# Kernel tuning notes

Hardware: AMD Instinct MI355X
Metric: run time of the kernel (lower is better)

## Reference

```python
import jax, jax.numpy as jnp
import numpy as np

N, E = 100000, 1600000
IN, HID, NCLS = 128, 128, 64


def setup_inputs() -> dict:
    key = jax.random.key(0)
    ks = jax.random.split(key, 8)
    x = jax.random.normal(ks[0], (N, IN), jnp.float32)
    edge_index = jax.random.randint(ks[1], (2, E), 0, N, dtype=jnp.int32)
    s1 = 1.0 / np.sqrt(IN)
    s2 = 1.0 / np.sqrt(HID)
    return {
        "x": x,
        "edge_index": edge_index,
        "Wl1": jax.random.uniform(ks[2], (IN, HID), jnp.float32, -s1, s1),
        "Wr1": jax.random.uniform(ks[3], (IN, HID), jnp.float32, -s1, s1),
        "b1": jnp.zeros((HID,), jnp.float32),
        "Wl2": jax.random.uniform(ks[4], (HID, NCLS), jnp.float32, -s2, s2),
        "Wr2": jax.random.uniform(ks[5], (HID, NCLS), jnp.float32, -s2, s2),
        "b2": jnp.zeros((NCLS,), jnp.float32),
    }


def _sage_conv(x, src, dst, inv_deg, Wl, Wr, b):
    # mean-aggregate neighbor features at each destination node (PyG SAGEConv)
    agg = jax.ops.segment_sum(x[src], dst, num_segments=N)  # [N, d]
    agg = agg * inv_deg[:, None]
    # out = lin_l(mean_j x_j) + lin_r(x_i); bias lives in lin_l
    return agg @ Wl + x @ Wr + b


def reference(x, edge_index, Wl1, Wr1, b1, Wl2, Wr2, b2):
    src, dst = edge_index[0], edge_index[1]
    deg = jax.ops.segment_sum(jnp.ones((E,), jnp.float32), dst, num_segments=N)
    inv_deg = 1.0 / jnp.maximum(deg, 1.0)
    h = _sage_conv(x, src, dst, inv_deg, Wl1, Wr1, b1)
    h = jax.nn.relu(h)
    # dropout is identity at inference (training=False)
    h = _sage_conv(h, src, dst, inv_deg, Wl2, Wr2, b2)
    return jax.nn.log_softmax(h, axis=1)
```

## Files before the change

kernel.cpp:

```cpp
#include <hip/hip_runtime.h>
#include <hip/hip_bf16.h>


typedef __attribute__((ext_vector_type(8))) short short8;
typedef __attribute__((ext_vector_type(4))) float f32x4;
typedef __attribute__((ext_vector_type(2))) float f32x2;

#define NPB 512
#define BCAP 16384
#define CHUNK 8192

__device__ __forceinline__ ushort f2bf(float f) {
    unsigned u = __float_as_uint(f);
    return (ushort)((u + 0x7fff + ((u >> 16) & 1)) >> 16);
}
__device__ __forceinline__ float bflo(unsigned v) { return __uint_as_float(v << 16); }
__device__ __forceinline__ float bfhi(unsigned v) { return __uint_as_float(v & 0xffff0000u); }
__device__ __forceinline__ unsigned pk4bf(float a, float b) {
    unsigned r;
    asm("v_cvt_pk_bf16_f32 %0, %1, %2" : "=v"(r) : "v"(a), "v"(b));
    return r;
}
__device__ __forceinline__ f32x2 shflx2(f32x2 v, int m) {
    f32x2 r; r[0] = __shfl_xor(v[0], m); r[1] = __shfl_xor(v[1], m); return r;
}

__device__ __forceinline__ void wfrag_one(const float* W, ushort* Wf, int i, int COLS) {
    int j = i & 7, m = (i >> 3) & 15, kc = (i >> 7) & 15, ct = i >> 11;
    Wf[i] = f2bf(W[(kc * 8 + j) * COLS + ct * 16 + m]);
}

__global__ void __launch_bounds__(256)
k1_scatter_cvtw(const int* __restrict__ src, const int* __restrict__ dst,
                int* __restrict__ bcount, unsigned* __restrict__ bbuf, int E, int NSC,
                const float* __restrict__ Wl1, const float* __restrict__ Wr1,
                const float* __restrict__ Wl2, const float* __restrict__ Wr2,
                ushort* __restrict__ Wf_l1, ushort* __restrict__ Wf_r1,
                ushort* __restrict__ Wf_l2, ushort* __restrict__ Wf_r2) {
    int tid = threadIdx.x;
    if ((int)blockIdx.x >= NSC) {
        int i = ((int)blockIdx.x - NSC) * 256 + tid;
        if (i < 16384)       wfrag_one(Wl1, Wf_l1, i, 128);
        else if (i < 32768)  wfrag_one(Wr1, Wf_r1, i - 16384, 128);
        else if (i < 40960)  wfrag_one(Wl2, Wf_l2, i - 32768, 64);
        else if (i < 49152)  wfrag_one(Wr2, Wf_r2, i - 40960, 64);
        return;
    }
    __shared__ unsigned entry[CHUNK];
    __shared__ unsigned char ebkt[CHUNK];
    __shared__ int lhist[256], lbase[256], lcur[256];
    lhist[tid] = 0;
    __syncthreads();
    int e0 = blockIdx.x * CHUNK;
    int cnt = min(CHUNK, E - e0);
    int nv = cnt >> 2;
    for (int t = tid; t < nv; t += 256) {
        int4 d4 = ((const int4*)(dst + e0))[t];
        int4 s4 = ((const int4*)(src + e0))[t];
        int i = t * 4;
        int b0 = d4.x >> 9, b1 = d4.y >> 9, b2 = d4.z >> 9, b3 = d4.w >> 9;
        entry[i + 0] = ((unsigned)s4.x << 9) | (unsigned)(d4.x & 511);
        entry[i + 1] = ((unsigned)s4.y << 9) | (unsigned)(d4.y & 511);
        entry[i + 2] = ((unsigned)s4.z << 9) | (unsigned)(d4.z & 511);
        entry[i + 3] = ((unsigned)s4.w << 9) | (unsigned)(d4.w & 511);
        ebkt[i + 0] = (unsigned char)b0; ebkt[i + 1] = (unsigned char)b1;
        ebkt[i + 2] = (unsigned char)b2; ebkt[i + 3] = (unsigned char)b3;
        atomicAdd(&lhist[b0], 1); atomicAdd(&lhist[b1], 1);
        atomicAdd(&lhist[b2], 1); atomicAdd(&lhist[b3], 1);
    }
    for (int i = (nv << 2) + tid; i < cnt; i += 256) {
        int d = dst[e0 + i], s = src[e0 + i];
        int b = d >> 9;
        entry[i] = ((unsigned)s << 9) | (unsigned)(d & 511);
        ebkt[i] = (unsigned char)b;
        atomicAdd(&lhist[b], 1);
    }
    __syncthreads();
    int h = lhist[tid];
    lbase[tid] = (h > 0) ? atomicAdd(&bcount[tid], h) : 0;
    lcur[tid] = 0;
    __syncthreads();
    for (int i = tid; i < cnt; i += 256) {
        int b = ebkt[i];
        int o = atomicAdd(&lcur[b], 1);
        bbuf[(long)b * BCAP + lbase[b] + o] = entry[i];
    }
}

template <int CTOT>
__device__ __forceinline__ void stage_weights(const ushort* __restrict__ Wfl,
                                              const ushort* __restrict__ Wfr,
                                              ushort* dst, int tid) {
    constexpr int HALF = CTOT / 2;
    constexpr int ITERS = (CTOT * 2) / 8192;
#pragma unroll
    for (int r = 0; r < ITERS; ++r) {
        int u = r * 4096 + tid * 8;
        const ushort* s = (u < HALF) ? (Wfl + u) : (Wfr + (u - HALF));
        *(short8*)(dst + u) = *(const short8*)s;
    }
}

template <int COLS, bool F32IN>
__device__ __forceinline__ void proj_body(int bid, int tid,
                            const void* __restrict__ xin,
                            const ushort* __restrict__ Wfl, const ushort* __restrict__ Wfr,
                            const float* __restrict__ bias,
                            unsigned char* __restrict__ p8, ushort* __restrict__ q, int N,
                            ushort* wsm) {
    constexpr int CT = COLS / 16;
    stage_weights<2 * COLS * 128>(Wfl, Wfr, wsm, tid);
    __syncthreads();
    const ushort* Wl = wsm;
    const ushort* Wr = wsm + COLS * 128;

    int wave = tid >> 6, lane = tid & 63;
    int quad = lane >> 4, m = lane & 15;
    long row0 = (long)bid * 128 + wave * 16;
    long node = row0 + m;
    long arow = (node < N) ? node : (N - 1);

    f32x4 accp[CT], accq[CT];
#pragma unroll
    for (int ct = 0; ct < CT; ++ct) { accp[ct] = (f32x4)0.0f; accq[ct] = (f32x4)0.0f; }

#pragma unroll
    for (int kk = 0; kk < 128; kk += 32) {
        short8 b;
        if (F32IN) {
            const float* xf = (const float*)xin + arow * 128 + kk + quad * 8;
            float4 f0 = *(const float4*)xf;
            float4 f1 = *(const float4*)(xf + 4);
            union { short8 s; unsigned u[4]; } bu;
            bu.u[0] = pk4bf(f0.x, f0.y);
            bu.u[1] = pk4bf(f0.z, f0.w);
            bu.u[2] = pk4bf(f1.x, f1.y);
            bu.u[3] = pk4bf(f1.z, f1.w);
            b = bu.s;
        } else {
            b = *(const short8*)((const ushort*)xin + arow * 128 + kk + quad * 8);
        }
        int kc = (kk >> 3) + quad;
#pragma unroll
        for (int ct = 0; ct < CT; ++ct) {
            int boff = ((ct * 16 + kc) * 16 + m) * 8;
            short8 al = *(const short8*)(Wl + boff);
            short8 ar = *(const short8*)(Wr + boff);
            accp[ct] = __builtin_amdgcn_mfma_f32_16x16x32_bf16(al, b, accp[ct], 0, 0, 0);
            accq[ct] = __builtin_amdgcn_mfma_f32_16x16x32_bf16(ar, b, accq[ct], 0, 0, 0);
        }
    }

    if (node <= N) {
        unsigned msk = (node == N) ? 0u : ~0u;
#pragma unroll
        for (int ct = 0; ct < CT; ++ct) {
            int c0 = ct * 16 + quad * 4;
            float4 bv = *(const float4*)(bias + c0);
            float q0 = accq[ct][0] + bv.x, q1 = accq[ct][1] + bv.y;
            float q2 = accq[ct][2] + bv.z, q3 = accq[ct][3] + bv.w;
            unsigned w = (unsigned)__builtin_amdgcn_cvt_pk_fp8_f32(accp[ct][0], accp[ct][1], 0, false);
            w = (unsigned)__builtin_amdgcn_cvt_pk_fp8_f32(accp[ct][2], accp[ct][3], (int)w, true);
            *(unsigned*)(p8 + node * COLS + c0) = w & msk;
            uint2 qw; qw.x = pk4bf(q0, q1) & msk; qw.y = pk4bf(q2, q3) & msk;
            *(uint2*)(q + node * COLS + c0) = qw;
        }
    }
}

__global__ void __launch_bounds__(512, 4)
k2_csr_proj1(const unsigned* __restrict__ bbuf, const int* __restrict__ bcount,
             int* __restrict__ rsd,
             float* __restrict__ inv_deg, int* __restrict__ ssrc, int NBcsr, int N,
             const float* __restrict__ x,
             const ushort* __restrict__ Wfl, const ushort* __restrict__ Wfr,
             const float* __restrict__ bias,
             unsigned char* __restrict__ p8, ushort* __restrict__ q) {
    extern __shared__ char smem[];
    int tid = threadIdx.x;
    if ((int)blockIdx.x >= NBcsr) {
        proj_body<128, true>((int)blockIdx.x - NBcsr, tid, x, Wfl, Wfr, bias, p8, q, N,
                             (ushort*)smem);
        return;
    }
    int* sdeg = (int*)smem;
    int* lcur = sdeg + NPB;
    int* wsum = lcur + NPB;
    unsigned* ecache = (unsigned*)(wsum + 16);
    const int ECAPV = 3836;
    int b = blockIdx.x;
    int node0 = b * NPB;
    sdeg[tid] = 0;
    __syncthreads();
    int cnt = bcount[b];
    long base = (long)b * BCAP;
    const unsigned* bb = bbuf + base;
    int nv = cnt >> 2;
    int cnv = min(nv, ECAPV);
    for (int t = tid; t < nv; t += 512) {
        uint4 e = ((const uint4*)bb)[t];
        if (t < cnv) ((uint4*)ecache)[t] = e;
        atomicAdd(&sdeg[e.x & 511], 1);
        atomicAdd(&sdeg[e.y & 511], 1);
        atomicAdd(&sdeg[e.z & 511], 1);
        atomicAdd(&sdeg[e.w & 511], 1);
    }
    for (int i = (nv << 2) + tid; i < cnt; i += 512)
        atomicAdd(&sdeg[bb[i] & 511], 1);
    __syncthreads();
    int lane = tid & 63, wv = tid >> 6;
    int c0 = sdeg[tid];
    int dp = (c0 + 15) & ~15;
    int v = dp;
#pragma unroll
    for (int o = 1; o < 64; o <<= 1) {
        int t = __shfl_up(v, o);
        if (lane >= o) v += t;
    }
    if (lane == 63) wsum[wv] = v;
    __syncthreads();
    int add = 0;
    for (int w = 0; w < wv; ++w) add += wsum[w];
    int rs0 = v + add - dp;
    lcur[tid] = rs0;
    if (node0 + tid < N) {
        int2 rv; rv.x = (int)(base + rs0); rv.y = dp;
        *(int2*)(rsd + 2 * (node0 + tid)) = rv;
        inv_deg[node0 + tid] = 1.0f / (float)(c0 > 1 ? c0 : 1);
    }
    __syncthreads();
    for (int t = tid; t < cnv; t += 512) {
        uint4 e = ((const uint4*)ecache)[t];
        int p0 = atomicAdd(&lcur[e.x & 511], 1);
        int p1 = atomicAdd(&lcur[e.y & 511], 1);
        int p2 = atomicAdd(&lcur[e.z & 511], 1);
        int p3 = atomicAdd(&lcur[e.w & 511], 1);
        ssrc[base + p0] = (int)(e.x >> 9);
        ssrc[base + p1] = (int)(e.y >> 9);
        ssrc[base + p2] = (int)(e.z >> 9);
        ssrc[base + p3] = (int)(e.w >> 9);
    }
    for (int t = cnv + tid; t < nv; t += 512) {
        uint4 e = ((const uint4*)bb)[t];
        int p0 = atomicAdd(&lcur[e.x & 511], 1);
        int p1 = atomicAdd(&lcur[e.y & 511], 1);
        int p2 = atomicAdd(&lcur[e.z & 511], 1);
        int p3 = atomicAdd(&lcur[e.w & 511], 1);
        ssrc[base + p0] = (int)(e.x >> 9);
        ssrc[base + p1] = (int)(e.y >> 9);
        ssrc[base + p2] = (int)(e.z >> 9);
        ssrc[base + p3] = (int)(e.w >> 9);
    }
    for (int i = (nv << 2) + tid; i < cnt; i += 512) {
        unsigned w = bb[i];
        int pos = atomicAdd(&lcur[w & 511], 1);
        ssrc[base + pos] = (int)(w >> 9);
    }
    for (int i = c0; i < dp; ++i) ssrc[base + rs0 + i] = N;
    if (tid == 511) {
        int tot = v + add;
        for (int k = 0; k < 16; ++k) ssrc[base + tot + k] = N;
    }
}

__global__ void __launch_bounds__(256)
agg_relu_kernel(const unsigned char* __restrict__ p8,
                const ushort* __restrict__ q,
                const int* __restrict__ ssrc,
                const int* __restrict__ rsd,
                const float* __restrict__ inv_deg,
                ushort* __restrict__ hb, int N) {
    int wave = threadIdx.x >> 6, lane = threadIdx.x & 63;
    int nA = blockIdx.x * 8 + wave * 2;
    if (nA >= N) return;
    int nB = nA + 1;
    bool hasB = (nB < N);
    int g = lane >> 4, lm = lane & 15;
    int2 rvA = *(const int2*)(rsd + 2 * nA);
    int2 rvB = hasB ? *(const int2*)(rsd + 2 * nB) : make_int2(rvA.x, 0);
    int dpA = rvA.y, dpB = rvB.y;
    float ivA = inv_deg[nA];
    float ivB = hasB ? inv_deg[nB] : 0.f;
    uint4 qvA = make_uint4(0u,0u,0u,0u), qvB = make_uint4(0u,0u,0u,0u);
    if (g == 0) {
        qvA = *(const uint4*)(q + (long)nA * 128 + lm * 8);
        if (hasB) qvB = *(const uint4*)(q + (long)nB * 128 + lm * 8);
    }
    const int* spA = ssrc + rvA.x;
    const int* spB = ssrc + rvB.x;
    const unsigned char* pb = p8 + lm * 8;
    f32x2 aA0=(f32x2)0.f, aA1=(f32x2)0.f, aA2=(f32x2)0.f, aA3=(f32x2)0.f;
    f32x2 aB0=(f32x2)0.f, aB1=(f32x2)0.f, aB2=(f32x2)0.f, aB3=(f32x2)0.f;
    int4 sA = *(const int4*)(spA + 4 * g);
    int4 sB = *(const int4*)(spB + 4 * g);
    int dmin = min(dpA, dpB);
    int j = 0;
    for (; j < dmin; j += 16) {
        uint2 a0 = *(const uint2*)(pb + (unsigned)sA.x * 128u);
        uint2 a1 = *(const uint2*)(pb + (unsigned)sA.y * 128u);
        uint2 a2 = *(const uint2*)(pb + (unsigned)sA.z * 128u);
        uint2 a3 = *(const uint2*)(pb + (unsigned)sA.w * 128u);
        uint2 b0 = *(const uint2*)(pb + (unsigned)sB.x * 128u);
        uint2 b1 = *(const uint2*)(pb + (unsigned)sB.y * 128u);
        uint2 b2 = *(const uint2*)(pb + (unsigned)sB.z * 128u);
        uint2 b3 = *(const uint2*)(pb + (unsigned)sB.w * 128u);
        sA = *(const int4*)(spA + j + 16 + 4 * g);
        sB = *(const int4*)(spB + j + 16 + 4 * g);
        aA0 += __builtin_amdgcn_cvt_pk_f32_fp8((int)a0.x, false);
        aA1 += __builtin_amdgcn_cvt_pk_f32_fp8((int)a0.x, true);
        aA2 += __builtin_amdgcn_cvt_pk_f32_fp8((int)a0.y, false);
        aA3 += __builtin_amdgcn_cvt_pk_f32_fp8((int)a0.y, true);
        aA0 += __builtin_amdgcn_cvt_pk_f32_fp8((int)a1.x, false);
        aA1 += __builtin_amdgcn_cvt_pk_f32_fp8((int)a1.x, true);
        aA2 += __builtin_amdgcn_cvt_pk_f32_fp8((int)a1.y, false);
        aA3 += __builtin_amdgcn_cvt_pk_f32_fp8((int)a1.y, true);
        aA0 += __builtin_amdgcn_cvt_pk_f32_fp8((int)a2.x, false);
        aA1 += __builtin_amdgcn_cvt_pk_f32_fp8((int)a2.x, true);
        aA2 += __builtin_amdgcn_cvt_pk_f32_fp8((int)a2.y, false);
        aA3 += __builtin_amdgcn_cvt_pk_f32_fp8((int)a2.y, true);
        aA0 += __builtin_amdgcn_cvt_pk_f32_fp8((int)a3.x, false);
        aA1 += __builtin_amdgcn_cvt_pk_f32_fp8((int)a3.x, true);
        aA2 += __builtin_amdgcn_cvt_pk_f32_fp8((int)a3.y, false);
        aA3 += __builtin_amdgcn_cvt_pk_f32_fp8((int)a3.y, true);
        aB0 += __builtin_amdgcn_cvt_pk_f32_fp8((int)b0.x, false);
        aB1 += __builtin_amdgcn_cvt_pk_f32_fp8((int)b0.x, true);
        aB2 += __builtin_amdgcn_cvt_pk_f32_fp8((int)b0.y, false);
        aB3 += __builtin_amdgcn_cvt_pk_f32_fp8((int)b0.y, true);
        aB0 += __builtin_amdgcn_cvt_pk_f32_fp8((int)b1.x, false);
        aB1 += __builtin_amdgcn_cvt_pk_f32_fp8((int)b1.x, true);
        aB2 += __builtin_amdgcn_cvt_pk_f32_fp8((int)b1.y, false);
        aB3 += __builtin_amdgcn_cvt_pk_f32_fp8((int)b1.y, true);
        aB0 += __builtin_amdgcn_cvt_pk_f32_fp8((int)b2.x, false);
        aB1 += __builtin_amdgcn_cvt_pk_f32_fp8((int)b2.x, true);
        aB2 += __builtin_amdgcn_cvt_pk_f32_fp8((int)b2.y, false);
        aB3 += __builtin_amdgcn_cvt_pk_f32_fp8((int)b2.y, true);
        aB0 += __builtin_amdgcn_cvt_pk_f32_fp8((int)b3.x, false);
        aB1 += __builtin_amdgcn_cvt_pk_f32_fp8((int)b3.x, true);
        aB2 += __builtin_amdgcn_cvt_pk_f32_fp8((int)b3.y, false);
        aB3 += __builtin_amdgcn_cvt_pk_f32_fp8((int)b3.y, true);
    }
    for (; j < dpA; j += 16) {
        uint2 a0 = *(const uint2*)(pb + (unsigned)sA.x * 128u);
        uint2 a1 = *(const uint2*)(pb + (unsigned)sA.y * 128u);
        uint2 a2 = *(const uint2*)(pb + (unsigned)sA.z * 128u);
        uint2 a3 = *(const uint2*)(pb + (unsigned)sA.w * 128u);
        sA = *(const int4*)(spA + j + 16 + 4 * g);
        aA0 += __builtin_amdgcn_cvt_pk_f32_fp8((int)a0.x, false);
        aA1 += __builtin_amdgcn_cvt_pk_f32_fp8((int)a0.x, true);
        aA2 += __builtin_amdgcn_cvt_pk_f32_fp8((int)a0.y, false);
        aA3 += __builtin_amdgcn_cvt_pk_f32_fp8((int)a0.y, true);
        aA0 += __builtin_amdgcn_cvt_pk_f32_fp8((int)a1.x, false);
        aA1 += __builtin_amdgcn_cvt_pk_f32_fp8((int)a1.x, true);
        aA2 += __builtin_amdgcn_cvt_pk_f32_fp8((int)a1.y, false);
        aA3 += __builtin_amdgcn_cvt_pk_f32_fp8((int)a1.y, true);
        aA0 += __builtin_amdgcn_cvt_pk_f32_fp8((int)a2.x, false);
        aA1 += __builtin_amdgcn_cvt_pk_f32_fp8((int)a2.x, true);
        aA2 += __builtin_amdgcn_cvt_pk_f32_fp8((int)a2.y, false);
        aA3 += __builtin_amdgcn_cvt_pk_f32_fp8((int)a2.y, true);
        aA0 += __builtin_amdgcn_cvt_pk_f32_fp8((int)a3.x, false);
        aA1 += __builtin_amdgcn_cvt_pk_f32_fp8((int)a3.x, true);
        aA2 += __builtin_amdgcn_cvt_pk_f32_fp8((int)a3.y, false);
        aA3 += __builtin_amdgcn_cvt_pk_f32_fp8((int)a3.y, true);
    }
    for (; j < dpB; j += 16) {
        uint2 b0 = *(const uint2*)(pb + (unsigned)sB.x * 128u);
        uint2 b1 = *(const uint2*)(pb + (unsigned)sB.y * 128u);
        uint2 b2 = *(const uint2*)(pb + (unsigned)sB.z * 128u);
        uint2 b3 = *(const uint2*)(pb + (unsigned)sB.w * 128u);
        sB = *(const int4*)(spB + j + 16 + 4 * g);
        aB0 += __builtin_amdgcn_cvt_pk_f32_fp8((int)b0.x, false);
        aB1 += __builtin_amdgcn_cvt_pk_f32_fp8((int)b0.x, true);
        aB2 += __builtin_amdgcn_cvt_pk_f32_fp8((int)b0.y, false);
        aB3 += __builtin_amdgcn_cvt_pk_f32_fp8((int)b0.y, true);
        aB0 += __builtin_amdgcn_cvt_pk_f32_fp8((int)b1.x, false);
        aB1 += __builtin_amdgcn_cvt_pk_f32_fp8((int)b1.x, true);
        aB2 += __builtin_amdgcn_cvt_pk_f32_fp8((int)b1.y, false);
        aB3 += __builtin_amdgcn_cvt_pk_f32_fp8((int)b1.y, true);
        aB0 += __builtin_amdgcn_cvt_pk_f32_fp8((int)b2.x, false);
        aB1 += __builtin_amdgcn_cvt_pk_f32_fp8((int)b2.x, true);
        aB2 += __builtin_amdgcn_cvt_pk_f32_fp8((int)b2.y, false);
        aB3 += __builtin_amdgcn_cvt_pk_f32_fp8((int)b2.y, true);
        aB0 += __builtin_amdgcn_cvt_pk_f32_fp8((int)b3.x, false);
        aB1 += __builtin_amdgcn_cvt_pk_f32_fp8((int)b3.x, true);
        aB2 += __builtin_amdgcn_cvt_pk_f32_fp8((int)b3.y, false);
        aB3 += __builtin_amdgcn_cvt_pk_f32_fp8((int)b3.y, true);
    }
    aA0 += shflx2(aA0, 16); aA1 += shflx2(aA1, 16);
    aA2 += shflx2(aA2, 16); aA3 += shflx2(aA3, 16);
    aB0 += shflx2(aB0, 16); aB1 += shflx2(aB1, 16);
    aB2 += shflx2(aB2, 16); aB3 += shflx2(aB3, 16);
    aA0 += shflx2(aA0, 32); aA1 += shflx2(aA1, 32);
    aA2 += shflx2(aA2, 32); aA3 += shflx2(aA3, 32);
    aB0 += shflx2(aB0, 32); aB1 += shflx2(aB1, 32);
    aB2 += shflx2(aB2, 32); aB3 += shflx2(aB3, 32);
    if (g == 0) {
        float h0 = fmaxf(aA0[0] * ivA + bflo(qvA.x), 0.f);
        float h1 = fmaxf(aA0[1] * ivA + bfhi(qvA.x), 0.f);
        float h2 = fmaxf(aA1[0] * ivA + bflo(qvA.y), 0.f);
        float h3 = fmaxf(aA1[1] * ivA + bfhi(qvA.y), 0.f);
        float h4 = fmaxf(aA2[0] * ivA + bflo(qvA.z), 0.f);
        float h5 = fmaxf(aA2[1] * ivA + bfhi(qvA.z), 0.f);
        float h6 = fmaxf(aA3[0] * ivA + bflo(qvA.w), 0.f);
        float h7 = fmaxf(aA3[1] * ivA + bfhi(qvA.w), 0.f);
        uint4 hw;
        hw.x = pk4bf(h0, h1); hw.y = pk4bf(h2, h3);
        hw.z = pk4bf(h4, h5); hw.w = pk4bf(h6, h7);
        *(uint4*)(hb + (long)nA * 128 + lm * 8) = hw;
        if (hasB) {
            float g0 = fmaxf(aB0[0] * ivB + bflo(qvB.x), 0.f);
            float g1 = fmaxf(aB0[1] * ivB + bfhi(qvB.x), 0.f);
            float g2 = fmaxf(aB1[0] * ivB + bflo(qvB.y), 0.f);
            float g3 = fmaxf(aB1[1] * ivB + bfhi(qvB.y), 0.f);
            float g4 = fmaxf(aB2[0] * ivB + bflo(qvB.z), 0.f);
            float g5 = fmaxf(aB2[1] * ivB + bfhi(qvB.z), 0.f);
            float g6 = fmaxf(aB3[0] * ivB + bflo(qvB.w), 0.f);
            float g7 = fmaxf(aB3[1] * ivB + bfhi(qvB.w), 0.f);
            uint4 gw;
            gw.x = pk4bf(g0, g1); gw.y = pk4bf(g2, g3);
            gw.z = pk4bf(g4, g5); gw.w = pk4bf(g6, g7);
            *(uint4*)(hb + (long)nB * 128 + lm * 8) = gw;
        }
    }
}

__global__ void __launch_bounds__(512, 4)
proj2_kernel(const ushort* __restrict__ hb,
             const ushort* __restrict__ Wfl, const ushort* __restrict__ Wfr,
             const float* __restrict__ bias,
             unsigned char* __restrict__ u8, ushort* __restrict__ v, int N) {
    __shared__ ushort wsm[2 * 64 * 128];
    proj_body<64, false>((int)blockIdx.x, (int)threadIdx.x, hb, Wfl, Wfr, bias, u8, v, N,
                         wsm);
}

__global__ void __launch_bounds__(256)
agg_lsm_kernel(const unsigned char* __restrict__ u8,
               const ushort* __restrict__ v,
               const int* __restrict__ ssrc,
               const int* __restrict__ rsd,
               const float* __restrict__ inv_deg,
               float* __restrict__ out, int N) {
    int wave = threadIdx.x >> 6, lane = threadIdx.x & 63;
    int nA = blockIdx.x * 8 + wave * 2;
    if (nA >= N) return;
    int nB = nA + 1;
    bool hasB = (nB < N);
    int g = lane >> 4, lm = lane & 15;
    int2 rvA = *(const int2*)(rsd + 2 * nA);
    int2 rvB = hasB ? *(const int2*)(rsd + 2 * nB) : make_int2(rvA.x, 0);
    int dpA = rvA.y, dpB = rvB.y;
    float ivA = inv_deg[nA];
    float ivB = hasB ? inv_deg[nB] : 0.f;
    uint2 vvA = *(const uint2*)(v + (long)nA * 64 + lm * 4);
    uint2 vvB = hasB ? *(const uint2*)(v + (long)nB * 64 + lm * 4) : make_uint2(0u,0u);
    const int* spA = ssrc + rvA.x;
    const int* spB = ssrc + rvB.x;
    const unsigned char* ub = u8 + lm * 4;
    f32x2 aA0=(f32x2)0.f, aA1=(f32x2)0.f, aB0=(f32x2)0.f, aB1=(f32x2)0.f;
    int4 sA = *(const int4*)(spA + 4 * g);
    int4 sB = *(const int4*)(spB + 4 * g);
    int dmin = min(dpA, dpB);
    int j = 0;
    for (; j < dmin; j += 16) {
        unsigned a0 = *(const unsigned*)(ub + (unsigned)sA.x * 64u);
        unsigned a1 = *(const unsigned*)(ub + (unsigned)sA.y * 64u);
        unsigned a2 = *(const unsigned*)(ub + (unsigned)sA.z * 64u);
        unsigned a3 = *(const unsigned*)(ub + (unsigned)sA.w * 64u);
        unsigned b0 = *(const unsigned*)(ub + (unsigned)sB.x * 64u);
        unsigned b1 = *(const unsigned*)(ub + (unsigned)sB.y * 64u);
        unsigned b2 = *(const unsigned*)(ub + (unsigned)sB.z * 64u);
        unsigned b3 = *(const unsigned*)(ub + (unsigned)sB.w * 64u);
        sA = *(const int4*)(spA + j + 16 + 4 * g);
        sB = *(const int4*)(spB + j + 16 + 4 * g);
        aA0 += __builtin_amdgcn_cvt_pk_f32_fp8((int)a0, false);
        aA1 += __builtin_amdgcn_cvt_pk_f32_fp8((int)a0, true);
        aA0 += __builtin_amdgcn_cvt_pk_f32_fp8((int)a1, false);
        aA1 += __builtin_amdgcn_cvt_pk_f32_fp8((int)a1, true);
        aA0 += __builtin_amdgcn_cvt_pk_f32_fp8((int)a2, false);
        aA1 += __builtin_amdgcn_cvt_pk_f32_fp8((int)a2, true);
        aA0 += __builtin_amdgcn_cvt_pk_f32_fp8((int)a3, false);
        aA1 += __builtin_amdgcn_cvt_pk_f32_fp8((int)a3, true);
        aB0 += __builtin_amdgcn_cvt_pk_f32_fp8((int)b0, false);
        aB1 += __builtin_amdgcn_cvt_pk_f32_fp8((int)b0, true);
        aB0 += __builtin_amdgcn_cvt_pk_f32_fp8((int)b1, false);
        aB1 += __builtin_amdgcn_cvt_pk_f32_fp8((int)b1, true);
        aB0 += __builtin_amdgcn_cvt_pk_f32_fp8((int)b2, false);
        aB1 += __builtin_amdgcn_cvt_pk_f32_fp8((int)b2, true);
        aB0 += __builtin_amdgcn_cvt_pk_f32_fp8((int)b3, false);
        aB1 += __builtin_amdgcn_cvt_pk_f32_fp8((int)b3, true);
    }
    for (; j < dpA; j += 16) {
        unsigned a0 = *(const unsigned*)(ub + (unsigned)sA.x * 64u);
        unsigned a1 = *(const unsigned*)(ub + (unsigned)sA.y * 64u);
        unsigned a2 = *(const unsigned*)(ub + (unsigned)sA.z * 64u);
        unsigned a3 = *(const unsigned*)(ub + (unsigned)sA.w * 64u);
        sA = *(const int4*)(spA + j + 16 + 4 * g);
        aA0 += __builtin_amdgcn_cvt_pk_f32_fp8((int)a0, false);
        aA1 += __builtin_amdgcn_cvt_pk_f32_fp8((int)a0, true);
        aA0 += __builtin_amdgcn_cvt_pk_f32_fp8((int)a1, false);
        aA1 += __builtin_amdgcn_cvt_pk_f32_fp8((int)a1, true);
        aA0 += __builtin_amdgcn_cvt_pk_f32_fp8((int)a2, false);
        aA1 += __builtin_amdgcn_cvt_pk_f32_fp8((int)a2, true);
        aA0 += __builtin_amdgcn_cvt_pk_f32_fp8((int)a3, false);
        aA1 += __builtin_amdgcn_cvt_pk_f32_fp8((int)a3, true);
    }
    for (; j < dpB; j += 16) {
        unsigned b0 = *(const unsigned*)(ub + (unsigned)sB.x * 64u);
        unsigned b1 = *(const unsigned*)(ub + (unsigned)sB.y * 64u);
        unsigned b2 = *(const unsigned*)(ub + (unsigned)sB.z * 64u);
        unsigned b3 = *(const unsigned*)(ub + (unsigned)sB.w * 64u);
        sB = *(const int4*)(spB + j + 16 + 4 * g);
        aB0 += __builtin_amdgcn_cvt_pk_f32_fp8((int)b0, false);
        aB1 += __builtin_amdgcn_cvt_pk_f32_fp8((int)b0, true);
        aB0 += __builtin_amdgcn_cvt_pk_f32_fp8((int)b1, false);
        aB1 += __builtin_amdgcn_cvt_pk_f32_fp8((int)b1, true);
        aB0 += __builtin_amdgcn_cvt_pk_f32_fp8((int)b2, false);
        aB1 += __builtin_amdgcn_cvt_pk_f32_fp8((int)b2, true);
        aB0 += __builtin_amdgcn_cvt_pk_f32_fp8((int)b3, false);
        aB1 += __builtin_amdgcn_cvt_pk_f32_fp8((int)b3, true);
    }
    aA0 += shflx2(aA0, 16); aA1 += shflx2(aA1, 16);
    aB0 += shflx2(aB0, 16); aB1 += shflx2(aB1, 16);
    aA0 += shflx2(aA0, 32); aA1 += shflx2(aA1, 32);
    aB0 += shflx2(aB0, 32); aB1 += shflx2(aB1, 32);

    float zA0 = aA0[0] * ivA + bflo(vvA.x), zA1 = aA0[1] * ivA + bfhi(vvA.x);
    float zA2 = aA1[0] * ivA + bflo(vvA.y), zA3 = aA1[1] * ivA + bfhi(vvA.y);
    float zB0 = aB0[0] * ivB + bflo(vvB.x), zB1 = aB0[1] * ivB + bfhi(vvB.x);
    float zB2 = aB1[0] * ivB + bflo(vvB.y), zB3 = aB1[1] * ivB + bfhi(vvB.y);
    float mA = fmaxf(fmaxf(zA0, zA1), fmaxf(zA2, zA3));
    float mB = fmaxf(fmaxf(zB0, zB1), fmaxf(zB2, zB3));
#pragma unroll
    for (int o = 8; o > 0; o >>= 1) {
        mA = fmaxf(mA, __shfl_xor(mA, o));
        mB = fmaxf(mB, __shfl_xor(mB, o));
    }
    float eA = (__expf(zA0 - mA) + __expf(zA1 - mA)) + (__expf(zA2 - mA) + __expf(zA3 - mA));
    float eB = (__expf(zB0 - mB) + __expf(zB1 - mB)) + (__expf(zB2 - mB) + __expf(zB3 - mB));
#pragma unroll
    for (int o = 8; o > 0; o >>= 1) {
        eA += __shfl_xor(eA, o);
        eB += __shfl_xor(eB, o);
    }
    float lsA = mA + __logf(eA);
    float lsB = mB + __logf(eB);
    if (g == 0) {
        float4 oA;
        oA.x = zA0 - lsA; oA.y = zA1 - lsA; oA.z = zA2 - lsA; oA.w = zA3 - lsA;
        *(float4*)(out + (long)nA * 64 + lm * 4) = oA;
        if (hasB) {
            float4 oB;
            oB.x = zB0 - lsB; oB.y = zB1 - lsB; oB.z = zB2 - lsB; oB.w = zB3 - lsB;
            *(float4*)(out + (long)nB * 64 + lm * 4) = oB;
        }
    }
}

extern "C" void kernel_launch(void* const* d_in, const int* in_sizes, int n_in,
                              void* d_out, int out_size, void* d_ws, size_t ws_size,
                              hipStream_t stream) {
    const float* x   = (const float*)d_in[0];
    const int*   ei  = (const int*)d_in[1];
    const float* Wl1 = (const float*)d_in[2];
    const float* Wr1 = (const float*)d_in[3];
    const float* b1  = (const float*)d_in[4];
    const float* Wl2 = (const float*)d_in[5];
    const float* Wr2 = (const float*)d_in[6];
    const float* b2  = (const float*)d_in[7];

    const int N = in_sizes[0] / 128;
    const int E = in_sizes[1] / 2;
    const int* src = ei;
    const int* dst = ei + E;
    const int NB = (N + NPB - 1) / NPB;
    const int NSC = (E + CHUNK - 1) / CHUNK;

    size_t off = 0;
    auto take = [&](size_t nbytes) -> void* {
        void* ptr = (void*)((char*)d_ws + off);
        off += (nbytes + 255) & ~(size_t)255;
        return ptr;
    };
    int*      bcount    = (int*)take((size_t)NB * 4);
    unsigned* bbuf      = (unsigned*)take((size_t)NB * BCAP * 4);
    int*      rsd       = (int*)take((size_t)N * 8);
    float*    inv_deg   = (float*)take((size_t)N * 4);
    int*      ssrc      = (int*)take((size_t)NB * BCAP * 4);
    unsigned char* p8   = (unsigned char*)take((size_t)(N + 1) * 128);
    ushort*   q         = (ushort*)take((size_t)(N + 1) * 128 * 2);
    ushort*   hb        = (ushort*)take((size_t)N * 128 * 2);
    ushort*   Wf_l1     = (ushort*)take(128 * 128 * 2);
    ushort*   Wf_r1     = (ushort*)take(128 * 128 * 2);
    ushort*   Wf_l2     = (ushort*)take(64 * 128 * 2);
    ushort*   Wf_r2     = (ushort*)take(64 * 128 * 2);
    unsigned char* u8 = p8;
    ushort*        v  = q;
    (void)ws_size; (void)n_in; (void)out_size;

    static bool attr_set = false;
    if (!attr_set) {
        hipFuncSetAttribute((const void*)k2_csr_proj1,
                            hipFuncAttributeMaxDynamicSharedMemorySize, 65536);
        attr_set = true;
    }

    hipMemsetAsync(bcount, 0, (size_t)NB * 4, stream);

    k1_scatter_cvtw<<<NSC + 192, 256, 0, stream>>>(src, dst, bcount, bbuf, E, NSC,
                                                   Wl1, Wr1, Wl2, Wr2,
                                                   Wf_l1, Wf_r1, Wf_l2, Wf_r2);

    int P1 = (N + 127) / 128;
    k2_csr_proj1<<<NB + P1, 512, 65536, stream>>>(bbuf, bcount, rsd, inv_deg,
                                                  ssrc, NB, N, x, Wf_l1, Wf_r1, b1, p8, q);

    agg_relu_kernel<<<(N + 7) / 8, 256, 0, stream>>>(p8, q, ssrc, rsd, inv_deg, hb, N);

    proj2_kernel<<<(N + 127) / 128, 512, 0, stream>>>(hb, Wf_l2, Wf_r2, b2, u8, v, N);
    agg_lsm_kernel<<<(N + 7) / 8, 256, 0, stream>>>(u8, v, ssrc, rsd, inv_deg,
                                                    (float*)d_out, N);
}
```

Before: 242.4 us.

## Fuse layer-1 aggregation with layer-2 projection and persist proj1 tiles

Merges the ReLU aggregation kernel with the second-layer projection. Each 512-thread block aggregates 16 nodes into shared memory and runs the bf16 MFMA for both weight matrices directly, so the hb intermediate never goes through global memory and one launch disappears. The layer-1 projection blocks become a persistent grid of 316 that stages the weights once and loops over tiles. The final aggregation now handles one node per wave instead of two. The trade-off is that weights are restaged into shared memory in every small fused block, and occupancy is lower because of the shared-memory footprint.

```diff
diff --git a/kernel.cpp b/kernel.cpp
--- a/kernel.cpp
+++ b/kernel.cpp
@@ -102,18 +102,12 @@
 }
 
 template <int COLS, bool F32IN>
-__device__ __forceinline__ void proj_body(int bid, int tid,
+__device__ __forceinline__ void proj_tile(int bid, int tid,
                             const void* __restrict__ xin,
-                            const ushort* __restrict__ Wfl, const ushort* __restrict__ Wfr,
+                            const ushort* Wl, const ushort* Wr,
                             const float* __restrict__ bias,
-                            unsigned char* __restrict__ p8, ushort* __restrict__ q, int N,
-                            ushort* wsm) {
+                            unsigned char* __restrict__ p8, ushort* __restrict__ q, int N) {
     constexpr int CT = COLS / 16;
-    stage_weights<2 * COLS * 128>(Wfl, Wfr, wsm, tid);
-    __syncthreads();
-    const ushort* Wl = wsm;
-    const ushort* Wr = wsm + COLS * 128;
-
     int wave = tid >> 6, lane = tid & 63;
     int quad = lane >> 4, m = lane & 15;
     long row0 = (long)bid * 128 + wave * 16;
@@ -171,7 +165,8 @@
 __global__ void __launch_bounds__(512, 4)
 k2_csr_proj1(const unsigned* __restrict__ bbuf, const int* __restrict__ bcount,
              int* __restrict__ rsd,
-             float* __restrict__ inv_deg, int* __restrict__ ssrc, int NBcsr, int N,
+             float* __restrict__ inv_deg, int* __restrict__ ssrc,
+             int NBcsr, int PGRID, int NT, int N,
              const float* __restrict__ x,
              const ushort* __restrict__ Wfl, const ushort* __restrict__ Wfr,
              const float* __restrict__ bias,
@@ -179,8 +174,11 @@
     extern __shared__ char smem[];
     int tid = threadIdx.x;
     if ((int)blockIdx.x >= NBcsr) {
-        proj_body<128, true>((int)blockIdx.x - NBcsr, tid, x, Wfl, Wfr, bias, p8, q, N,
-                             (ushort*)smem);
+        ushort* wsm = (ushort*)smem;
+        stage_weights<2 * 128 * 128>(Wfl, Wfr, wsm, tid);
+        __syncthreads();
+        for (int t = (int)blockIdx.x - NBcsr; t < NT; t += PGRID)
+            proj_tile<128, true>(t, tid, x, wsm, wsm + 128 * 128, bias, p8, q, N);
         return;
     }
     int* sdeg = (int*)smem;
@@ -263,28 +261,36 @@
     }
 }
 
-__global__ void __launch_bounds__(256)
-agg_relu_kernel(const unsigned char* __restrict__ p8,
-                const ushort* __restrict__ q,
-                const int* __restrict__ ssrc,
-                const int* __restrict__ rsd,
-                const float* __restrict__ inv_deg,
-                ushort* __restrict__ hb, int N) {
-    int wave = threadIdx.x >> 6, lane = threadIdx.x & 63;
-    int nA = blockIdx.x * 8 + wave * 2;
-    if (nA >= N) return;
-    int nB = nA + 1;
-    bool hasB = (nB < N);
+__global__ void __launch_bounds__(512, 6)
+agg_relu_proj2(const unsigned char* __restrict__ p8,
+               const ushort* __restrict__ q,
+               const int* __restrict__ ssrc,
+               const int* __restrict__ rsd,
+               const float* __restrict__ inv_deg,
+               const ushort* __restrict__ Wfl, const ushort* __restrict__ Wfr,
+               const float* __restrict__ bias,
+               unsigned char* __restrict__ u8,
+               ushort* __restrict__ v,
+               int N) {
+    __shared__ ushort wsm[2 * 64 * 128];
+    __shared__ ushort hs[16][136];
+    int tid = threadIdx.x;
+    stage_weights<2 * 64 * 128>(Wfl, Wfr, wsm, tid);
+
+    int wave = tid >> 6, lane = tid & 63;
+    int row0 = (int)blockIdx.x * 16;
+    int nA = row0 + wave * 2, nB = nA + 1;
+    int cA = (nA < N) ? nA : N - 1;
+    int cB = (nB < N) ? nB : N - 1;
     int g = lane >> 4, lm = lane & 15;
-    int2 rvA = *(const int2*)(rsd + 2 * nA);
-    int2 rvB = hasB ? *(const int2*)(rsd + 2 * nB) : make_int2(rvA.x, 0);
+    int2 rvA = *(const int2*)(rsd + 2 * cA);
+    int2 rvB = *(const int2*)(rsd + 2 * cB);
     int dpA = rvA.y, dpB = rvB.y;
-    float ivA = inv_deg[nA];
-    float ivB = hasB ? inv_deg[nB] : 0.f;
+    float ivA = inv_deg[cA], ivB = inv_deg[cB];
     uint4 qvA = make_uint4(0u,0u,0u,0u), qvB = make_uint4(0u,0u,0u,0u);
     if (g == 0) {
-        qvA = *(const uint4*)(q + (long)nA * 128 + lm * 8);
-        if (hasB) qvB = *(const uint4*)(q + (long)nB * 128 + lm * 8);
+        qvA = *(const uint4*)(q + (long)cA * 128 + lm * 8);
+        qvB = *(const uint4*)(q + (long)cB * 128 + lm * 8);
     }
     const int* spA = ssrc + rvA.x;
     const int* spB = ssrc + rvB.x;
@@ -402,35 +408,53 @@
         float h5 = fmaxf(aA2[1] * ivA + bfhi(qvA.z), 0.f);
         float h6 = fmaxf(aA3[0] * ivA + bflo(qvA.w), 0.f);
         float h7 = fmaxf(aA3[1] * ivA + bfhi(qvA.w), 0.f);
-        uint4 hw;
-        hw.x = pk4bf(h0, h1); hw.y = pk4bf(h2, h3);
-        hw.z = pk4bf(h4, h5); hw.w = pk4bf(h6, h7);
-        *(uint4*)(hb + (long)nA * 128 + lm * 8) = hw;
-        if (hasB) {
-            float g0 = fmaxf(aB0[0] * ivB + bflo(qvB.x), 0.f);
-            float g1 = fmaxf(aB0[1] * ivB + bfhi(qvB.x), 0.f);
-            float g2 = fmaxf(aB1[0] * ivB + bflo(qvB.y), 0.f);
-            float g3 = fmaxf(aB1[1] * ivB + bfhi(qvB.y), 0.f);
-            float g4 = fmaxf(aB2[0] * ivB + bflo(qvB.z), 0.f);
-            float g5 = fmaxf(aB2[1] * ivB + bfhi(qvB.z), 0.f);
-            float g6 = fmaxf(aB3[0] * ivB + bflo(qvB.w), 0.f);
-            float g7 = fmaxf(aB3[1] * ivB + bfhi(qvB.w), 0.f);
-            uint4 gw;
-            gw.x = pk4bf(g0, g1); gw.y = pk4bf(g2, g3);
-            gw.z = pk4bf(g4, g5); gw.w = pk4bf(g6, g7);
-            *(uint4*)(hb + (long)nB * 128 + lm * 8) = gw;
+        uint4 hwA;
+        hwA.x = pk4bf(h0, h1); hwA.y = pk4bf(h2, h3);
+        hwA.z = pk4bf(h4, h5); hwA.w = pk4bf(h6, h7);
+        *(uint4*)(&hs[wave * 2 + 0][lm * 8]) = hwA;
+        float g0 = fmaxf(aB0[0] * ivB + bflo(qvB.x), 0.f);
+        float g1 = fmaxf(aB0[1] * ivB + bfhi(qvB.x), 0.f);
+        float g2 = fmaxf(aB1[0] * ivB + bflo(qvB.y), 0.f);
+        float g3 = fmaxf(aB1[1] * ivB + bfhi(qvB.y), 0.f);
+        float g4 = fmaxf(aB2[0] * ivB + bflo(qvB.z), 0.f);
+        float g5 = fmaxf(aB2[1] * ivB + bfhi(qvB.z), 0.f);
+        float g6 = fmaxf(aB3[0] * ivB + bflo(qvB.w), 0.f);
+        float g7 = fmaxf(aB3[1] * ivB + bfhi(qvB.w), 0.f);
+        uint4 hwB;
+        hwB.x = pk4bf(g0, g1); hwB.y = pk4bf(g2, g3);
+        hwB.z = pk4bf(g4, g5); hwB.w = pk4bf(g6, g7);
+        *(uint4*)(&hs[wave * 2 + 1][lm * 8]) = hwB;
+    }
+    __syncthreads();
+    {
+        int mat = wave & 1, ct = wave >> 1;
+        const ushort* W = mat ? (wsm + 64 * 128) : wsm;
+        f32x4 acc = (f32x4)0.0f;
+#pragma unroll
+        for (int kk = 0; kk < 128; kk += 32) {
+            short8 bfr = *(const short8*)(&hs[lm][kk + g * 8]);
+            int kc = (kk >> 3) + g;
+            short8 afr = *(const short8*)(W + ((ct * 16 + kc) * 16 + lm) * 8);
+            acc = __builtin_amdgcn_mfma_f32_16x16x32_bf16(afr, bfr, acc, 0, 0, 0);
         }
-    }
-}
-
-__global__ void __launch_bounds__(512, 4)
-proj2_kernel(const ushort* __restrict__ hb,
-             const ushort* __restrict__ Wfl, const ushort* __restrict__ Wfr,
-             const float* __restrict__ bias,
-             unsigned char* __restrict__ u8, ushort* __restrict__ v, int N) {
-    __shared__ ushort wsm[2 * 64 * 128];
-    proj_body<64, false>((int)blockIdx.x, (int)threadIdx.x, hb, Wfl, Wfr, bias, u8, v, N,
-                         wsm);
+        int node = row0 + lm;
+        if (node < N) {
+            int c0 = ct * 16 + g * 4;
+            if (mat == 0) {
+                unsigned w = (unsigned)__builtin_amdgcn_cvt_pk_fp8_f32(acc[0], acc[1], 0, false);
+                w = (unsigned)__builtin_amdgcn_cvt_pk_fp8_f32(acc[2], acc[3], (int)w, true);
+                *(unsigned*)(u8 + (long)node * 64 + c0) = w;
+            } else {
+                float4 bv = *(const float4*)(bias + c0);
+                uint2 qw;
+                qw.x = pk4bf(acc[0] + bv.x, acc[1] + bv.y);
+                qw.y = pk4bf(acc[2] + bv.z, acc[3] + bv.w);
+                *(uint2*)(v + (long)node * 64 + c0) = qw;
+            }
+        }
+    }
+    if (blockIdx.x == 0 && tid < 16)
+        ((unsigned*)(u8 + (long)N * 64))[tid] = 0u;
 }
 
 __global__ void __launch_bounds__(256)
@@ -441,118 +465,48 @@
                const float* __restrict__ inv_deg,
                float* __restrict__ out, int N) {
     int wave = threadIdx.x >> 6, lane = threadIdx.x & 63;
-    int nA = blockIdx.x * 8 + wave * 2;
-    if (nA >= N) return;
-    int nB = nA + 1;
-    bool hasB = (nB < N);
+    int n = blockIdx.x * 4 + wave;
+    if (n >= N) return;
     int g = lane >> 4, lm = lane & 15;
-    int2 rvA = *(const int2*)(rsd + 2 * nA);
-    int2 rvB = hasB ? *(const int2*)(rsd + 2 * nB) : make_int2(rvA.x, 0);
-    int dpA = rvA.y, dpB = rvB.y;
-    float ivA = inv_deg[nA];
-    float ivB = hasB ? inv_deg[nB] : 0.f;
-    uint2 vvA = *(const uint2*)(v + (long)nA * 64 + lm * 4);
-    uint2 vvB = hasB ? *(const uint2*)(v + (long)nB * 64 + lm * 4) : make_uint2(0u,0u);
-    const int* spA = ssrc + rvA.x;
-    const int* spB = ssrc + rvB.x;
+    int2 rv = *(const int2*)(rsd + 2 * n);
+    int start = rv.x, dp = rv.y;
+    float iv = inv_deg[n];
+    uint2 vv2 = *(const uint2*)(v + (long)n * 64 + lm * 4);
+    const int* sp = ssrc + start;
     const unsigned char* ub = u8 + lm * 4;
-    f32x2 aA0=(f32x2)0.f, aA1=(f32x2)0.f, aB0=(f32x2)0.f, aB1=(f32x2)0.f;
-    int4 sA = *(const int4*)(spA + 4 * g);
-    int4 sB = *(const int4*)(spB + 4 * g);
-    int dmin = min(dpA, dpB);
-    int j = 0;
-    for (; j < dmin; j += 16) {
-        unsigned a0 = *(const unsigned*)(ub + (unsigned)sA.x * 64u);
-        unsigned a1 = *(const unsigned*)(ub + (unsigned)sA.y * 64u);
-        unsigned a2 = *(const unsigned*)(ub + (unsigned)sA.z * 64u);
-        unsigned a3 = *(const unsigned*)(ub + (unsigned)sA.w * 64u);
-        unsigned b0 = *(const unsigned*)(ub + (unsigned)sB.x * 64u);
-        unsigned b1 = *(const unsigned*)(ub + (unsigned)sB.y * 64u);
-        unsigned b2 = *(const unsigned*)(ub + (unsigned)sB.z * 64u);
-        unsigned b3 = *(const unsigned*)(ub + (unsigned)sB.w * 64u);
-        sA = *(const int4*)(spA + j + 16 + 4 * g);
-        sB = *(const int4*)(spB + j + 16 + 4 * g);
-        aA0 += __builtin_amdgcn_cvt_pk_f32_fp8((int)a0, false);
-        aA1 += __builtin_amdgcn_cvt_pk_f32_fp8((int)a0, true);
-        aA0 += __builtin_amdgcn_cvt_pk_f32_fp8((int)a1, false);
-        aA1 += __builtin_amdgcn_cvt_pk_f32_fp8((int)a1, true);
-        aA0 += __builtin_amdgcn_cvt_pk_f32_fp8((int)a2, false);
-        aA1 += __builtin_amdgcn_cvt_pk_f32_fp8((int)a2, true);
-        aA0 += __builtin_amdgcn_cvt_pk_f32_fp8((int)a3, false);
-        aA1 += __builtin_amdgcn_cvt_pk_f32_fp8((int)a3, true);
-        aB0 += __builtin_amdgcn_cvt_pk_f32_fp8((int)b0, false);
-        aB1 += __builtin_amdgcn_cvt_pk_f32_fp8((int)b0, true);
-        aB0 += __builtin_amdgcn_cvt_pk_f32_fp8((int)b1, false);
-        aB1 += __builtin_amdgcn_cvt_pk_f32_fp8((int)b1, true);
-        aB0 += __builtin_amdgcn_cvt_pk_f32_fp8((int)b2, false);
-        aB1 += __builtin_amdgcn_cvt_pk_f32_fp8((int)b2, true);
-        aB0 += __builtin_amdgcn_cvt_pk_f32_fp8((int)b3, false);
-        aB1 += __builtin_amdgcn_cvt_pk_f32_fp8((int)b3, true);
-    }
-    for (; j < dpA; j += 16) {
-        unsigned a0 = *(const unsigned*)(ub + (unsigned)sA.x * 64u);
-        unsigned a1 = *(const unsigned*)(ub + (unsigned)sA.y * 64u);
-        unsigned a2 = *(const unsigned*)(ub + (unsigned)sA.z * 64u);
-        unsigned a3 = *(const unsigned*)(ub + (unsigned)sA.w * 64u);
-        sA = *(const int4*)(spA + j + 16 + 4 * g);
-        aA0 += __builtin_amdgcn_cvt_pk_f32_fp8((int)a0, false);
-        aA1 += __builtin_amdgcn_cvt_pk_f32_fp8((int)a0, true);
-        aA0 += __builtin_amdgcn_cvt_pk_f32_fp8((int)a1, false);
-        aA1 += __builtin_amdgcn_cvt_pk_f32_fp8((int)a1, true);
-        aA0 += __builtin_amdgcn_cvt_pk_f32_fp8((int)a2, false);
-        aA1 += __builtin_amdgcn_cvt_pk_f32_fp8((int)a2, true);
-        aA0 += __builtin_amdgcn_cvt_pk_f32_fp8((int)a3, false);
-        aA1 += __builtin_amdgcn_cvt_pk_f32_fp8((int)a3, true);
-    }
-    for (; j < dpB; j += 16) {
-        unsigned b0 = *(const unsigned*)(ub + (unsigned)sB.x * 64u);
-        unsigned b1 = *(const unsigned*)(ub + (unsigned)sB.y * 64u);
-        unsigned b2 = *(const unsigned*)(ub + (unsigned)sB.z * 64u);
-        unsigned b3 = *(const unsigned*)(ub + (unsigned)sB.w * 64u);
-        sB = *(const int4*)(spB + j + 16 + 4 * g);
-        aB0 += __builtin_amdgcn_cvt_pk_f32_fp8((int)b0, false);
-        aB1 += __builtin_amdgcn_cvt_pk_f32_fp8((int)b0, true);
-        aB0 += __builtin_amdgcn_cvt_pk_f32_fp8((int)b1, false);
-        aB1 += __builtin_amdgcn_cvt_pk_f32_fp8((int)b1, true);
-        aB0 += __builtin_amdgcn_cvt_pk_f32_fp8((int)b2, false);
-        aB1 += __builtin_amdgcn_cvt_pk_f32_fp8((int)b2, true);
-        aB0 += __builtin_amdgcn_cvt_pk_f32_fp8((int)b3, false);
-        aB1 += __builtin_amdgcn_cvt_pk_f32_fp8((int)b3, true);
-    }
-    aA0 += shflx2(aA0, 16); aA1 += shflx2(aA1, 16);
-    aB0 += shflx2(aB0, 16); aB1 += shflx2(aB1, 16);
-    aA0 += shflx2(aA0, 32); aA1 += shflx2(aA1, 32);
-    aB0 += shflx2(aB0, 32); aB1 += shflx2(aB1, 32);
-
-    float zA0 = aA0[0] * ivA + bflo(vvA.x), zA1 = aA0[1] * ivA + bfhi(vvA.x);
-    float zA2 = aA1[0] * ivA + bflo(vvA.y), zA3 = aA1[1] * ivA + bfhi(vvA.y);
-    float zB0 = aB0[0] * ivB + bflo(vvB.x), zB1 = aB0[1] * ivB + bfhi(vvB.x);
-    float zB2 = aB1[0] * ivB + bflo(vvB.y), zB3 = aB1[1] * ivB + bfhi(vvB.y);
-    float mA = fmaxf(fmaxf(zA0, zA1), fmaxf(zA2, zA3));
-    float mB = fmaxf(fmaxf(zB0, zB1), fmaxf(zB2, zB3));
-#pragma unroll
-    for (int o = 8; o > 0; o >>= 1) {
-        mA = fmaxf(mA, __shfl_xor(mA, o));
-        mB = fmaxf(mB, __shfl_xor(mB, o));
-    }
-    float eA = (__expf(zA0 - mA) + __expf(zA1 - mA)) + (__expf(zA2 - mA) + __expf(zA3 - mA));
-    float eB = (__expf(zB0 - mB) + __expf(zB1 - mB)) + (__expf(zB2 - mB) + __expf(zB3 - mB));
-#pragma unroll
-    for (int o = 8; o > 0; o >>= 1) {
-        eA += __shfl_xor(eA, o);
-        eB += __shfl_xor(eB, o);
-    }
-    float lsA = mA + __logf(eA);
-    float lsB = mB + __logf(eB);
+    f32x2 a0 = (f32x2)0.f, a1 = (f32x2)0.f;
+    int4 s = *(const int4*)(sp + 4 * g);
+    for (int j = 0; j < dp; j += 16) {
+        unsigned v0 = *(const unsigned*)(ub + (unsigned)s.x * 64u);
+        unsigned v1 = *(const unsigned*)(ub + (unsigned)s.y * 64u);
+        unsigned v2 = *(const unsigned*)(ub + (unsigned)s.z * 64u);
+        unsigned v3 = *(const unsigned*)(ub + (unsigned)s.w * 64u);
+        s = *(const int4*)(sp + j + 16 + 4 * g);
+        a0 += __builtin_amdgcn_cvt_pk_f32_fp8((int)v0, false);
+        a1 += __builtin_amdgcn_cvt_pk_f32_fp8((int)v0, true);
+        a0 += __builtin_amdgcn_cvt_pk_f32_fp8((int)v1, false);
+        a1 += __builtin_amdgcn_cvt_pk_f32_fp8((int)v1, true);
+        a0 += __builtin_amdgcn_cvt_pk_f32_fp8((int)v2, false);
+        a1 += __builtin_amdgcn_cvt_pk_f32_fp8((int)v2, true);
+        a0 += __builtin_amdgcn_cvt_pk_f32_fp8((int)v3, false);
+        a1 += __builtin_amdgcn_cvt_pk_f32_fp8((int)v3, true);
+    }
+    a0 += shflx2(a0, 16); a1 += shflx2(a1, 16);
+    a0 += shflx2(a0, 32); a1 += shflx2(a1, 32);
+
+    float z0 = a0[0] * iv + bflo(vv2.x), z1 = a0[1] * iv + bfhi(vv2.x);
+    float z2 = a1[0] * iv + bflo(vv2.y), z3 = a1[1] * iv + bfhi(vv2.y);
+    float mx = fmaxf(fmaxf(z0, z1), fmaxf(z2, z3));
+#pragma unroll
+    for (int o = 8; o > 0; o >>= 1) mx = fmaxf(mx, __shfl_xor(mx, o));
+    float e = (__expf(z0 - mx) + __expf(z1 - mx)) + (__expf(z2 - mx) + __expf(z3 - mx));
+#pragma unroll
+    for (int o = 8; o > 0; o >>= 1) e += __shfl_xor(e, o);
+    float ls = mx + __logf(e);
     if (g == 0) {
-        float4 oA;
-        oA.x = zA0 - lsA; oA.y = zA1 - lsA; oA.z = zA2 - lsA; oA.w = zA3 - lsA;
-        *(float4*)(out + (long)nA * 64 + lm * 4) = oA;
-        if (hasB) {
-            float4 oB;
-            oB.x = zB0 - lsB; oB.y = zB1 - lsB; oB.z = zB2 - lsB; oB.w = zB3 - lsB;
-            *(float4*)(out + (long)nB * 64 + lm * 4) = oB;
-        }
+        float4 o0;
+        o0.x = z0 - ls; o0.y = z1 - ls; o0.z = z2 - ls; o0.w = z3 - ls;
+        *(float4*)(out + (long)n * 64 + lm * 4) = o0;
     }
 }
 
@@ -588,13 +542,12 @@
     int*      ssrc      = (int*)take((size_t)NB * BCAP * 4);
     unsigned char* p8   = (unsigned char*)take((size_t)(N + 1) * 128);
     ushort*   q         = (ushort*)take((size_t)(N + 1) * 128 * 2);
-    ushort*   hb        = (ushort*)take((size_t)N * 128 * 2);
+    unsigned char* u8   = (unsigned char*)take((size_t)(N + 1) * 64);
+    ushort*   v         = (ushort*)take((size_t)N * 64 * 2);
     ushort*   Wf_l1     = (ushort*)take(128 * 128 * 2);
     ushort*   Wf_r1     = (ushort*)take(128 * 128 * 2);
     ushort*   Wf_l2     = (ushort*)take(64 * 128 * 2);
     ushort*   Wf_r2     = (ushort*)take(64 * 128 * 2);
-    unsigned char* u8 = p8;
-    ushort*        v  = q;
     (void)ws_size; (void)n_in; (void)out_size;
 
     static bool attr_set = false;
@@ -610,13 +563,15 @@
                                                    Wl1, Wr1, Wl2, Wr2,
                                                    Wf_l1, Wf_r1, Wf_l2, Wf_r2);
 
-    int P1 = (N + 127) / 128;
-    k2_csr_proj1<<<NB + P1, 512, 65536, stream>>>(bbuf, bcount, rsd, inv_deg,
-                                                  ssrc, NB, N, x, Wf_l1, Wf_r1, b1, p8, q);
-
-    agg_relu_kernel<<<(N + 7) / 8, 256, 0, stream>>>(p8, q, ssrc, rsd, inv_deg, hb, N);
-
-    proj2_kernel<<<(N + 127) / 128, 512, 0, stream>>>(hb, Wf_l2, Wf_r2, b2, u8, v, N);
-    agg_lsm_kernel<<<(N + 7) / 8, 256, 0, stream>>>(u8, v, ssrc, rsd, inv_deg,
+    const int PGRID = 316;
+    const int NT = (N + 127) / 128;
+    k2_csr_proj1<<<NB + PGRID, 512, 65536, stream>>>(bbuf, bcount, rsd, inv_deg, ssrc,
+                                                     NB, PGRID, NT, N, x,
+                                                     Wf_l1, Wf_r1, b1, p8, q);
+
+    agg_relu_proj2<<<(N + 15) / 16, 512, 0, stream>>>(p8, q, ssrc, rsd, inv_deg,
+                                                      Wf_l2, Wf_r2, b2, u8, v, N);
+
+    agg_lsm_kernel<<<(N + 3) / 4, 256, 0, stream>>>(u8, v, ssrc, rsd, inv_deg,
                                                     (float*)d_out, N);
 }
```

After: 245.0 us. About the same (+1.1%).
